# Optimization experiments

Hardware: AMD Instinct MI355X
Metric: run time of the kernel (lower is better)

The kernel has to match this reference:

```python
import jax, jax.numpy as jnp
import numpy as np
import math

B, S, D = 2, 8192, 1024
NW, SHIFT = 16, 256          # num_windows, shift_window
NH, DH = 16, 64              # heads = D // dim_head
DFF = 4 * D
EPS = 1e-6


def setup_inputs() -> dict:
    key = jax.random.key(0)
    ks = jax.random.split(key, 12)
    s = 1.0 / math.sqrt(D)
    return {
        "x": jax.random.normal(ks[0], (B, S, D), jnp.float32),
        "wq": jax.random.normal(ks[1], (D, NH * DH), jnp.float32) * s,
        "wk": jax.random.normal(ks[2], (D, NH * DH), jnp.float32) * s,
        "wv": jax.random.normal(ks[3], (D, NH * DH), jnp.float32) * s,
        "wo": jax.random.normal(ks[4], (NH * DH, D), jnp.float32) * s,
        "g_attn": jnp.ones((D,), jnp.float32),
        "g_ff": jnp.ones((D,), jnp.float32),
        "w1": jax.random.normal(ks[5], (D, DFF), jnp.float32) * s,
        "b1": jnp.zeros((DFF,), jnp.float32),
        "w2": jax.random.normal(ks[6], (DFF, D), jnp.float32) * (1.0 / math.sqrt(DFF)),
        "b2": jnp.zeros((D,), jnp.float32),
    }


def _rmsnorm(x, g):
    return x * g * jax.lax.rsqrt(jnp.mean(x * x, axis=-1, keepdims=True) + EPS)


def reference(x, wq, wk, wv, wo, g_attn, g_ff, w1, b1, w2, b2):
    skip = x
    h = _rmsnorm(x, g_attn)
    # shift (note: source rolls by -shift both before AND after attention)
    h = jnp.roll(h, -SHIFT, axis=1)
    # window partition: [B, NW, n, D]
    n = S // NW
    h = h.reshape(B, NW, n, D)
    q = (h @ wq).reshape(B, NW, n, NH, DH)
    k = (h @ wk).reshape(B, NW, n, NH, DH)
    v = (h @ wv).reshape(B, NW, n, NH, DH)
    scores = jnp.einsum('bwqhd,bwkhd->bwhqk', q, k) * (1.0 / math.sqrt(DH))
    a = jax.nn.softmax(scores, axis=-1)
    o = jnp.einsum('bwhqk,bwkhd->bwqhd', a, v).reshape(B, NW, n, NH * DH)
    o = (o @ wo).reshape(B, S, D)
    o = jnp.roll(o, -SHIFT, axis=1)  # faithful to source (rolls -shift again)
    x = o + skip
    skip = x
    h = _rmsnorm(x, g_ff)
    h = jax.nn.gelu(h @ w1 + b1) @ w2 + b2
    return h + skip
```

## Files before the change

### kernel.cpp

```cpp
#include <hip/hip_runtime.h>
#include <stdint.h>

#define S_LEN 8192
#define D_DIM 1024
#define SHIFT_W 256
#define NROWS 16384

typedef __bf16 bf16;
typedef __bf16 bf16x8 __attribute__((ext_vector_type(8)));
typedef __bf16 bf16x4 __attribute__((ext_vector_type(4)));
typedef float f32x4 __attribute__((ext_vector_type(4)));

typedef __attribute__((address_space(1))) const void gas_t;
typedef __attribute__((address_space(3))) void las_t;

__device__ __forceinline__ void load_lds16(const void* g, void* l) {
  __builtin_amdgcn_global_load_lds((gas_t*)g, (las_t*)l, 16, 0, 0);
}

__device__ __forceinline__ int xcd_swizzle(int orig, int nwg) {
  return (orig & 7) * (nwg >> 3) + (orig >> 3);
}

__global__ __launch_bounds__(256) void k_transpose_cvt(const float* __restrict__ in,
                                                       bf16* __restrict__ out,
                                                       int R, int C) {
  __shared__ float tile[32][33];
  int lx = threadIdx.x & 31, ly = threadIdx.x >> 5;
  int tc = blockIdx.x * 32, tr = blockIdx.y * 32;
#pragma unroll
  for (int i = 0; i < 4; i++)
    tile[ly + i * 8][lx] = in[(size_t)(tr + ly + i * 8) * C + tc + lx];
  __syncthreads();
#pragma unroll
  for (int i = 0; i < 4; i++)
    out[(size_t)(tc + ly + i * 8) * R + tr + lx] = (bf16)tile[lx][ly + i * 8];
}

__global__ __launch_bounds__(256) void k_rmsnorm(const float* __restrict__ x,
                                                 const float* __restrict__ g,
                                                 bf16* __restrict__ out, int shift) {
  int row = blockIdx.x;
  int b = row >> 13, r = row & (S_LEN - 1);
  int src = (b << 13) | ((r + shift) & (S_LEN - 1));
  int t = threadIdx.x;
  float4 v = *(const float4*)(x + (size_t)src * D_DIM + t * 4);
  float ss = v.x * v.x + v.y * v.y + v.z * v.z + v.w * v.w;
#pragma unroll
  for (int off = 32; off; off >>= 1) ss += __shfl_xor(ss, off);
  __shared__ float red[4];
  if ((t & 63) == 0) red[t >> 6] = ss;
  __syncthreads();
  ss = red[0] + red[1] + red[2] + red[3];
  float sc = rsqrtf(ss * (1.0f / D_DIM) + 1e-6f);
  float4 gv = *(const float4*)(g + t * 4);
  bf16x4 o;
  o[0] = (bf16)(v.x * gv.x * sc);
  o[1] = (bf16)(v.y * gv.y * sc);
  o[2] = (bf16)(v.z * gv.z * sc);
  o[3] = (bf16)(v.w * gv.w * sc);
  *(bf16x4*)(out + (size_t)row * D_DIM + t * 4) = o;
}

#define VM4 asm volatile("s_waitcnt vmcnt(4)" ::: "memory")
#define VM0 asm volatile("s_waitcnt vmcnt(0)" ::: "memory")
#define BAR __builtin_amdgcn_s_barrier()

#define STAGE(kbase, kk, dbuf)                                        \
  {                                                                   \
    const bf16* _ga = gAs + (kbase) + (kk) * 32;                      \
    const bf16* _gb = gBs + (kbase) + (kk) * 32;                      \
    char* _lb = smem + (dbuf) * 65536 + (kk) * 16384 + wv * 1024;     \
    load_lds16(_ga, _lb);                                             \
    load_lds16(_ga + 128 * (size_t)K, _lb + 8192);                    \
    load_lds16(_gb, _lb + 32768);                                     \
    load_lds16(_gb + 128 * (size_t)K, _lb + 40960);                   \
  }

#define LOAD_A(dst, mh, kkof, base)                                   \
  {                                                                   \
    _Pragma("unroll") for (int mf = 0; mf < 4; mf++)                  \
        dst[mf] = *(const bf16x8*)((base) + (kkof) + aBase + (mh) * 4096 + mf * 1024); \
  }
#define LOAD_B(dst, kkof, base)                                       \
  {                                                                   \
    _Pragma("unroll") for (int nf = 0; nf < 4; nf++)                  \
        dst[nf] = *(const bf16x8*)((base) + (kkof) + bBase + nf * 1024); \
  }
#define MFMA16(mh, A_, B_)                                            \
  {                                                                   \
    __builtin_amdgcn_s_setprio(1);                                    \
    _Pragma("unroll") for (int mf = 0; mf < 4; mf++)                  \
        _Pragma("unroll") for (int nf = 0; nf < 4; nf++)              \
            acc[(mh) * 4 + mf][nf] = __builtin_amdgcn_mfma_f32_16x16x32_bf16( \
                A_[mf], B_[nf], acc[(mh) * 4 + mf][nf], 0, 0, 0);     \
    __builtin_amdgcn_s_setprio(0);                                    \
  }

template <int EPI>
__global__ __launch_bounds__(512, 2) void k_gemm(const bf16* __restrict__ A,
                                                 const bf16* __restrict__ BT,
                                                 bf16* __restrict__ obf,
                                                 float* __restrict__ of32,
                                                 const float* __restrict__ bias,
                                                 const float* __restrict__ skip,
                                                 int K, int ldc) {
  extern __shared__ char smem[];
  const int tid = threadIdx.x;
  const int wv = tid >> 6, lane = tid & 63;
  const int lr = lane & 15, lg = lane >> 4;
  const int wm = wv >> 2, wn = wv & 3;

  const int NB = gridDim.x >> 6;
  const int xcd = blockIdx.x & 7;
  const int l = blockIdx.x >> 3;
  const int mb = ((xcd & 3) << 4) + (l & 15);
  const int nb = (xcd >> 2) * (NB >> 1) + (l >> 4);
  const int m0 = mb * 256, n0 = nb * 256;

  const int sr = ((tid >> 6) << 4) + ((tid >> 2) & 15);
  const int skoff = (((tid & 3) ^ ((tid >> 3) & 3)) << 3);
  const bf16* gAs = A + (size_t)(m0 + sr) * K + skoff;
  const bf16* gBs = BT + (size_t)(n0 + sr) * K + skoff;

  const int kchunk = (lg ^ ((lr >> 1) & 3)) << 4;
  const int aBase = wm * 8192 + lr * 64 + kchunk;
  const int bBase = 32768 + wn * 4096 + lr * 64 + kchunk;

  f32x4 acc[8][4] = {};
  const int nt = K >> 6;

  bf16x8 aX[4], aY[4], b0[4], b1[4];

  STAGE(0, 0, 0);
  STAGE(0, 1, 0);
  if (nt > 1) STAGE(64, 0, 1);
  VM4;
  BAR;
  LOAD_A(aX, 0, 0, smem);
  LOAD_B(b0, 0, smem);

  for (int t = 0; t < nt; ++t) {
    const char* Bc = smem + (size_t)((t & 1) * 65536);
    const char* Bn = smem + (size_t)(((t + 1) & 1) * 65536);
    LOAD_A(aY, 1, 0, Bc);
    if (t + 1 < nt) {
      STAGE((t + 1) << 6, 1, (t + 1) & 1);
      VM4;
    }
    BAR;
    MFMA16(0, aX, b0);
    LOAD_A(aX, 0, 16384, Bc);
    LOAD_B(b1, 16384, Bc);
    BAR;
    MFMA16(1, aY, b0);
    LOAD_A(aY, 1, 16384, Bc);
    if (t + 2 < nt) {
      STAGE((t + 2) << 6, 0, t & 1);
      VM4;
    } else if (t + 1 < nt) {
      VM0;
    }
    BAR;
    MFMA16(0, aX, b1);
    if (t + 1 < nt) {
      LOAD_A(aX, 0, 0, Bn);
      LOAD_B(b0, 0, Bn);
      BAR;
    }
    MFMA16(1, aY, b1);
  }

  float* lds_f = (float*)smem;
  const int erow = tid >> 3;
  const int ecol0 = (tid & 7) * 4;
#pragma unroll
  for (int mh = 0; mh < 2; mh++)
#pragma unroll
    for (int wmr = 0; wmr < 2; wmr++) {
      BAR;
      if (wm == wmr) {
#pragma unroll
        for (int mf = 0; mf < 4; mf++) {
          int lrow = mf * 16 + lg * 4;
#pragma unroll
          for (int nf = 0; nf < 4; nf++) {
            int lcol = wn * 64 + nf * 16 + lr;
#pragma unroll
            for (int ii = 0; ii < 4; ii++)
              lds_f[(lrow + ii) * 260 + lcol] = acc[mh * 4 + mf][nf][ii];
          }
        }
      }
      BAR;
      int gr = m0 + wmr * 128 + mh * 64 + erow;
      size_t orow;
      if constexpr (EPI == 1) {
        int b = gr >> 13, rr = gr & (S_LEN - 1);
        orow = (size_t)((b << 13) | ((rr - SHIFT_W) & (S_LEN - 1))) * ldc;
      } else {
        orow = (size_t)gr * ldc;
      }
#pragma unroll
      for (int j = 0; j < 8; j++) {
        f32x4 v = *(const f32x4*)&lds_f[erow * 260 + ecol0 + j * 32];
        int col = n0 + ecol0 + j * 32;
        if constexpr (EPI == 0) {
          bf16x4 o;
#pragma unroll
          for (int e = 0; e < 4; e++) o[e] = (bf16)v[e];
          *(bf16x4*)(obf + orow + col) = o;
        } else if constexpr (EPI == 1) {
          f32x4 s = *(const f32x4*)(skip + orow + col);
          f32x4 r = v + s;
          *(f32x4*)(of32 + orow + col) = r;
        } else if constexpr (EPI == 2) {
          f32x4 bi = *(const f32x4*)(bias + col);
          bf16x4 o;
#pragma unroll
          for (int e = 0; e < 4; e++) {
            float z = v[e] + bi[e];
            float u = 0.7978845608f * (z + 0.044715f * z * z * z);
            u = fminf(fmaxf(u, -15.f), 15.f);
            float ex = __expf(2.f * u);
            o[e] = (bf16)(0.5f * z * (1.f + (ex - 1.f) / (ex + 1.f)));
          }
          *(bf16x4*)(obf + orow + col) = o;
        } else {
          f32x4 bi = *(const f32x4*)(bias + col);
          f32x4 s = *(const f32x4*)(skip + orow + col);
          f32x4 r = v + bi + s;
          *(f32x4*)(of32 + orow + col) = r;
        }
      }
    }
}

__global__ __launch_bounds__(256) void k_attn(const bf16* __restrict__ qkv,
                                              bf16* __restrict__ out) {
  __shared__ __align__(16) char Qs[8192];
  __shared__ __align__(16) char Ks[8192];
  __shared__ __align__(16) char Vs[8192];
  __shared__ __align__(16) char Ps[4][2048];
  const int tid = threadIdx.x;
  const int wave = tid >> 6, lane = tid & 63;
  const int lr = lane & 15, lg = lane >> 4;
  const int bid = xcd_swizzle(blockIdx.x, gridDim.x);
  const int qt = bid & 7;
  const int h = (bid >> 3) & 15;
  const int bw = bid >> 7;
  const int rowbase = bw * 512;
  const int qrow0 = rowbase + qt * 64;

  {
    int r = tid >> 2, c0 = tid & 3;
    const bf16* src = qkv + (size_t)(qrow0 + r) * 3072 + h * 64;
#pragma unroll
    for (int j = 0; j < 2; j++) {
      int ch = c0 + j * 4;
      uint4 val = *(const uint4*)(src + ch * 8);
      int byte = (r * 128 + ch * 16) ^ ((r & 7) << 4);
      *(uint4*)(Qs + byte) = val;
    }
  }
  __syncthreads();
  bf16x8 qf[2];
  {
    int qr = wave * 16 + lr;
#pragma unroll
    for (int kk = 0; kk < 2; kk++) {
      int byte = (qr * 128 + (kk * 32 + lg * 8) * 2) ^ ((qr & 7) << 4);
      qf[kk] = *(const bf16x8*)(Qs + byte);
    }
  }

  f32x4 oacc[4] = {};
  float m_run = -__builtin_inff(), l_run = 0.f;

  for (int kt = 0; kt < 8; ++kt) {
    __syncthreads();
    {
      int r = tid >> 2, c0 = tid & 3;
      const bf16* ksrc = qkv + (size_t)(rowbase + kt * 64 + r) * 3072 + 1024 + h * 64;
      const bf16* vsrc = ksrc + 1024;
#pragma unroll
      for (int j = 0; j < 2; j++) {
        int ch = c0 + j * 4;
        uint4 val = *(const uint4*)(ksrc + ch * 8);
        int byte = (r * 128 + ch * 16) ^ ((r & 7) << 4);
        *(uint4*)(Ks + byte) = val;
      }
#pragma unroll
      for (int j = 0; j < 2; j++) {
        int ch = c0 + j * 4;
        bf16x8 vv = *(const bf16x8*)(vsrc + ch * 8);
#pragma unroll
        for (int e = 0; e < 8; e++) {
          int d = ch * 8 + e;
          int byte = (d * 128 + r * 2) ^ ((d & 7) << 4);
          *(bf16*)(Vs + byte) = vv[e];
        }
      }
    }
    __syncthreads();
    f32x4 sc[4] = {};
#pragma unroll
    for (int kk = 0; kk < 2; kk++)
#pragma unroll
      for (int mf = 0; mf < 4; mf++) {
        int kr = mf * 16 + lr;
        int byte = (kr * 128 + (kk * 32 + lg * 8) * 2) ^ ((kr & 7) << 4);
        bf16x8 kf = *(const bf16x8*)(Ks + byte);
        sc[mf] = __builtin_amdgcn_mfma_f32_16x16x32_bf16(kf, qf[kk], sc[mf], 0, 0, 0);
      }
    float mx = -__builtin_inff();
#pragma unroll
    for (int mf = 0; mf < 4; mf++)
#pragma unroll
      for (int i = 0; i < 4; i++) mx = fmaxf(mx, sc[mf][i]);
    mx = fmaxf(mx, __shfl_xor(mx, 16));
    mx = fmaxf(mx, __shfl_xor(mx, 32));
    float mnew = fmaxf(m_run, mx);
    float alpha = __expf(0.125f * (m_run - mnew));
    float lsum = 0.f;
    float ps[4][4];
#pragma unroll
    for (int mf = 0; mf < 4; mf++)
#pragma unroll
      for (int i = 0; i < 4; i++) {
        float p = __expf(0.125f * (sc[mf][i] - mnew));
        ps[mf][i] = p;
        lsum += p;
      }
    lsum += __shfl_xor(lsum, 16);
    lsum += __shfl_xor(lsum, 32);
    l_run = l_run * alpha + lsum;
    m_run = mnew;
#pragma unroll
    for (int dm = 0; dm < 4; dm++) oacc[dm] *= alpha;
#pragma unroll
    for (int mf = 0; mf < 4; mf++) {
      bf16x4 pv;
#pragma unroll
      for (int i = 0; i < 4; i++) pv[i] = (bf16)ps[mf][i];
      int byte = (lr * 128 + (mf * 16 + lg * 4) * 2) ^ ((lr & 7) << 4);
      *(bf16x4*)(Ps[wave] + byte) = pv;
    }
#pragma unroll
    for (int kk = 0; kk < 2; kk++) {
      int pbyte = (lr * 128 + (kk * 32 + lg * 8) * 2) ^ ((lr & 7) << 4);
      bf16x8 pf = *(const bf16x8*)(Ps[wave] + pbyte);
#pragma unroll
      for (int dm = 0; dm < 4; dm++) {
        int d = dm * 16 + lr;
        int byte = (d * 128 + (kk * 32 + lg * 8) * 2) ^ ((d & 7) << 4);
        bf16x8 vf = *(const bf16x8*)(Vs + byte);
        oacc[dm] = __builtin_amdgcn_mfma_f32_16x16x32_bf16(vf, pf, oacc[dm], 0, 0, 0);
      }
    }
  }
  float inv = 1.f / l_run;
  int rowq = qrow0 + wave * 16 + lr;
#pragma unroll
  for (int dm = 0; dm < 4; dm++) {
    bf16x4 ov;
#pragma unroll
    for (int i = 0; i < 4; i++) ov[i] = (bf16)(oacc[dm][i] * inv);
    *(bf16x4*)(out + (size_t)rowq * 1024 + h * 64 + dm * 16 + lg * 4) = ov;
  }
}

extern "C" void kernel_launch(void* const* d_in, const int* in_sizes, int n_in,
                              void* d_out, int out_size, void* d_ws, size_t ws_size,
                              hipStream_t stream) {
  const float* x = (const float*)d_in[0];
  const float* wq = (const float*)d_in[1];
  const float* wk = (const float*)d_in[2];
  const float* wv = (const float*)d_in[3];
  const float* wo = (const float*)d_in[4];
  const float* ga = (const float*)d_in[5];
  const float* gf = (const float*)d_in[6];
  const float* w1 = (const float*)d_in[7];
  const float* b1 = (const float*)d_in[8];
  const float* w2 = (const float*)d_in[9];
  const float* b2 = (const float*)d_in[10];
  float* out = (float*)d_out;

  char* ws = (char*)d_ws;
  const size_t MB = 1024 * 1024;
  bf16* wqkvT = (bf16*)(ws);
  bf16* woT = (bf16*)(ws + 6 * MB);
  bf16* w1T = (bf16*)(ws + 8 * MB);
  bf16* w2T = (bf16*)(ws + 16 * MB);
  float* x1 = (float*)(ws + 24 * MB);
  bf16* hbuf = (bf16*)(ws + 88 * MB);
  bf16* qkv = (bf16*)(ws + 120 * MB);
  bf16* mid = qkv;

  (void)hipFuncSetAttribute(reinterpret_cast<const void*>(&k_gemm<0>),
                            hipFuncAttributeMaxDynamicSharedMemorySize, 131072);
  (void)hipFuncSetAttribute(reinterpret_cast<const void*>(&k_gemm<1>),
                            hipFuncAttributeMaxDynamicSharedMemorySize, 131072);
  (void)hipFuncSetAttribute(reinterpret_cast<const void*>(&k_gemm<2>),
                            hipFuncAttributeMaxDynamicSharedMemorySize, 131072);
  (void)hipFuncSetAttribute(reinterpret_cast<const void*>(&k_gemm<3>),
                            hipFuncAttributeMaxDynamicSharedMemorySize, 131072);

  k_transpose_cvt<<<dim3(32, 32), 256, 0, stream>>>(wq, wqkvT, 1024, 1024);
  k_transpose_cvt<<<dim3(32, 32), 256, 0, stream>>>(wk, wqkvT + 1024 * 1024, 1024, 1024);
  k_transpose_cvt<<<dim3(32, 32), 256, 0, stream>>>(wv, wqkvT + 2 * 1024 * 1024, 1024, 1024);
  k_transpose_cvt<<<dim3(32, 32), 256, 0, stream>>>(wo, woT, 1024, 1024);
  k_transpose_cvt<<<dim3(128, 32), 256, 0, stream>>>(w1, w1T, 1024, 4096);
  k_transpose_cvt<<<dim3(32, 128), 256, 0, stream>>>(w2, w2T, 4096, 1024);

  k_rmsnorm<<<NROWS, 256, 0, stream>>>(x, ga, hbuf, SHIFT_W);
  k_gemm<0><<<64 * 12, 512, 131072, stream>>>(hbuf, wqkvT, qkv, nullptr, nullptr, nullptr, 1024, 3072);
  k_attn<<<4096, 256, 0, stream>>>(qkv, hbuf);
  k_gemm<1><<<64 * 4, 512, 131072, stream>>>(hbuf, woT, nullptr, x1, nullptr, x, 1024, 1024);
  k_rmsnorm<<<NROWS, 256, 0, stream>>>(x1, gf, hbuf, 0);
  k_gemm<2><<<64 * 16, 512, 131072, stream>>>(hbuf, w1T, mid, nullptr, b1, nullptr, 1024, 4096);
  k_gemm<3><<<64 * 4, 512, 131072, stream>>>(mid, w2T, nullptr, out, b2, x1, 4096, 1024);
}
```

Baseline: 659.8 us.

## Restructure GEMM main loop into 8-phase ping-pong schedule with split staging

Rewrites the bf16 GEMM mainloop so each iteration covers two K tiles, split into eight phases. Each phase issues its LDS fragment reads, one half-stage of global-to-LDS loads (A or B separately), and a 16-MFMA cluster, with barriers between phases. The XOR swizzle on LDS addresses is dropped in favour of a plain linear layout. The goal is finer interleaving of memory traffic with MFMA work, at the cost of many more barriers and possible LDS bank conflicts without the swizzle. The loop assumes an even number of K tiles.

Measured after the change: 659.8 us. About the same (-0.0%).

```diff
diff --git a/kernel.cpp b/kernel.cpp
--- a/kernel.cpp
+++ b/kernel.cpp
@@ -66,35 +66,32 @@
 #define VM0 asm volatile("s_waitcnt vmcnt(0)" ::: "memory")
 #define BAR __builtin_amdgcn_s_barrier()
 
-#define STAGE(kbase, kk, dbuf)                                        \
-  {                                                                   \
-    const bf16* _ga = gAs + (kbase) + (kk) * 32;                      \
-    const bf16* _gb = gBs + (kbase) + (kk) * 32;                      \
-    char* _lb = smem + (dbuf) * 65536 + (kk) * 16384 + wv * 1024;     \
-    load_lds16(_ga, _lb);                                             \
-    load_lds16(_ga + 128 * (size_t)K, _lb + 8192);                    \
-    load_lds16(_gb, _lb + 32768);                                     \
-    load_lds16(_gb + 128 * (size_t)K, _lb + 40960);                   \
-  }
-
-#define LOAD_A(dst, mh, kkof, base)                                   \
-  {                                                                   \
-    _Pragma("unroll") for (int mf = 0; mf < 4; mf++)                  \
-        dst[mf] = *(const bf16x8*)((base) + (kkof) + aBase + (mh) * 4096 + mf * 1024); \
-  }
-#define LOAD_B(dst, kkof, base)                                       \
-  {                                                                   \
-    _Pragma("unroll") for (int nf = 0; nf < 4; nf++)                  \
-        dst[nf] = *(const bf16x8*)((base) + (kkof) + bBase + nf * 1024); \
-  }
-#define MFMA16(mh, A_, B_)                                            \
-  {                                                                   \
-    __builtin_amdgcn_s_setprio(1);                                    \
-    _Pragma("unroll") for (int mf = 0; mf < 4; mf++)                  \
-        _Pragma("unroll") for (int nf = 0; nf < 4; nf++)              \
-            acc[(mh) * 4 + mf][nf] = __builtin_amdgcn_mfma_f32_16x16x32_bf16( \
-                A_[mf], B_[nf], acc[(mh) * 4 + mf][nf], 0, 0, 0);     \
-    __builtin_amdgcn_s_setprio(0);                                    \
+#define STAGE_H(isB, kc, t)                                               \
+  {                                                                       \
+    const bf16* _g = ((isB) ? gBs : gAs) + (size_t)(t) * 64 + (kc) * 32;  \
+    char* _lb = smem + ((t) & 1) * 65536 + (isB) * 32768 + (kc) * 16384 + tid * 16; \
+    load_lds16(_g, _lb);                                                  \
+    load_lds16(_g + 128 * (size_t)K, _lb + 8192);                         \
+  }
+
+#define LDA(dst, mq, kc, bufb)                                            \
+  {                                                                       \
+    _Pragma("unroll") for (int mf = 0; mf < 4; mf++)                      \
+        dst[mf] = *(const bf16x8*)(smem + (bufb) + (kc) * 16384 + aOff + (mq) * 4096 + mf * 1024); \
+  }
+#define LDB(dst, kc, bufb)                                                \
+  {                                                                       \
+    _Pragma("unroll") for (int nf = 0; nf < 4; nf++)                      \
+        dst[nf] = *(const bf16x8*)(smem + (bufb) + (kc) * 16384 + bOff + nf * 1024); \
+  }
+#define MFMA16(mq, A_, B_)                                                \
+  {                                                                       \
+    __builtin_amdgcn_s_setprio(1);                                        \
+    _Pragma("unroll") for (int mf = 0; mf < 4; mf++)                      \
+        _Pragma("unroll") for (int nf = 0; nf < 4; nf++)                  \
+            acc[(mq) * 4 + mf][nf] = __builtin_amdgcn_mfma_f32_16x16x32_bf16( \
+                A_[mf], B_[nf], acc[(mq) * 4 + mf][nf], 0, 0, 0);         \
+    __builtin_amdgcn_s_setprio(0);                                        \
   }
 
 template <int EPI>
@@ -118,57 +115,81 @@
   const int nb = (xcd >> 2) * (NB >> 1) + (l >> 4);
   const int m0 = mb * 256, n0 = nb * 256;
 
-  const int sr = ((tid >> 6) << 4) + ((tid >> 2) & 15);
-  const int skoff = (((tid & 3) ^ ((tid >> 3) & 3)) << 3);
-  const bf16* gAs = A + (size_t)(m0 + sr) * K + skoff;
-  const bf16* gBs = BT + (size_t)(n0 + sr) * K + skoff;
-
-  const int kchunk = (lg ^ ((lr >> 1) & 3)) << 4;
-  const int aBase = wm * 8192 + lr * 64 + kchunk;
-  const int bBase = 32768 + wn * 4096 + lr * 64 + kchunk;
+  const bf16* gAs = A + (size_t)(m0 + (tid >> 2)) * K + (tid & 3) * 8;
+  const bf16* gBs = BT + (size_t)(n0 + (tid >> 2)) * K + (tid & 3) * 8;
+
+  const int aOff = (wm * 128 + lr) * 64 + lg * 16;
+  const int bOff = 32768 + (wn * 64 + lr) * 64 + lg * 16;
 
   f32x4 acc[8][4] = {};
   const int nt = K >> 6;
-
-  bf16x8 aX[4], aY[4], b0[4], b1[4];
-
-  STAGE(0, 0, 0);
-  STAGE(0, 1, 0);
-  if (nt > 1) STAGE(64, 0, 1);
+  const int niter = nt >> 1;
+
+  bf16x8 a0[4], a1[4], b0[4], b1[4];
+
+  STAGE_H(0, 0, 0);
+  STAGE_H(1, 0, 0);
+  STAGE_H(0, 1, 0);
+  STAGE_H(1, 1, 0);
+  STAGE_H(0, 0, 1);
+  STAGE_H(1, 0, 1);
   VM4;
   BAR;
-  LOAD_A(aX, 0, 0, smem);
-  LOAD_B(b0, 0, smem);
-
-  for (int t = 0; t < nt; ++t) {
-    const char* Bc = smem + (size_t)((t & 1) * 65536);
-    const char* Bn = smem + (size_t)(((t + 1) & 1) * 65536);
-    LOAD_A(aY, 1, 0, Bc);
-    if (t + 1 < nt) {
-      STAGE((t + 1) << 6, 1, (t + 1) & 1);
+
+  for (int j = 0; j < niter; ++j) {
+    const int t1 = 2 * j + 1, t2 = 2 * j + 2, t3 = 2 * j + 3;
+    LDA(a0, 0, 0, 0);
+    LDB(b0, 0, 0);
+    STAGE_H(0, 1, t1);
+    BAR;
+    MFMA16(0, a0, b0);
+    BAR;
+    LDA(a1, 1, 0, 0);
+    STAGE_H(1, 1, t1);
+    BAR;
+    MFMA16(1, a1, b0);
+    BAR;
+    LDA(a0, 1, 1, 0);
+    LDB(b1, 1, 0);
+    if (t2 < nt) STAGE_H(0, 0, t2);
+    BAR;
+    MFMA16(1, a0, b1);
+    BAR;
+    LDA(a1, 0, 1, 0);
+    if (t2 < nt) {
+      STAGE_H(1, 0, t2);
       VM4;
-    }
-    BAR;
-    MFMA16(0, aX, b0);
-    LOAD_A(aX, 0, 16384, Bc);
-    LOAD_B(b1, 16384, Bc);
-    BAR;
-    MFMA16(1, aY, b0);
-    LOAD_A(aY, 1, 16384, Bc);
-    if (t + 2 < nt) {
-      STAGE((t + 2) << 6, 0, t & 1);
+    } else {
+      VM0;
+    }
+    BAR;
+    MFMA16(0, a1, b1);
+    BAR;
+    LDA(a0, 0, 0, 65536);
+    LDB(b0, 0, 65536);
+    if (t2 < nt) STAGE_H(0, 1, t2);
+    BAR;
+    MFMA16(0, a0, b0);
+    BAR;
+    LDA(a1, 1, 0, 65536);
+    if (t2 < nt) STAGE_H(1, 1, t2);
+    BAR;
+    MFMA16(1, a1, b0);
+    BAR;
+    LDA(a0, 1, 1, 65536);
+    LDB(b1, 1, 65536);
+    if (t3 < nt) STAGE_H(0, 0, t3);
+    BAR;
+    MFMA16(1, a0, b1);
+    BAR;
+    LDA(a1, 0, 1, 65536);
+    if (t3 < nt) {
+      STAGE_H(1, 0, t3);
       VM4;
-    } else if (t + 1 < nt) {
-      VM0;
-    }
-    BAR;
-    MFMA16(0, aX, b1);
-    if (t + 1 < nt) {
-      LOAD_A(aX, 0, 0, Bn);
-      LOAD_B(b0, 0, Bn);
-      BAR;
-    }
-    MFMA16(1, aY, b1);
+    }
+    BAR;
+    MFMA16(0, a1, b1);
+    BAR;
   }
 
   float* lds_f = (float*)smem;
@@ -178,7 +199,7 @@
   for (int mh = 0; mh < 2; mh++)
 #pragma unroll
     for (int wmr = 0; wmr < 2; wmr++) {
-      BAR;
+      __syncthreads();
       if (wm == wmr) {
 #pragma unroll
         for (int mf = 0; mf < 4; mf++) {
@@ -192,7 +213,7 @@
           }
         }
       }
-      BAR;
+      __syncthreads();
       int gr = m0 + wmr * 128 + mh * 64 + erow;
       size_t orow;
       if constexpr (EPI == 1) {
```
